# Performance work log

Measured on AMD Instinct MI355X. Metric: run time of the kernel, lower is better.

The kernel has to match this reference:

```python
import jax, jax.numpy as jnp
import numpy as np
import math
from itertools import permutations

B, C_IN, C_OUT, K, N, D, F_DIM = 2, 4, 8, 4, 224, 2, 128


def _make_perms(k):
    # [k!, k, k] permutation matrices, same ordering as itertools.permutations
    nP = math.factorial(k)
    perms = np.zeros((nP, k, k), dtype=np.float32)
    for c, p in enumerate(permutations(range(k))):
        perms[c, np.arange(k), np.array(p)] = 1.0
    return jnp.asarray(perms)


def setup_inputs() -> dict:
    key = jax.random.key(0)
    ks = jax.random.split(key, 6)
    graph = jax.random.normal(ks[0], (B, C_IN, N, N), jnp.float32)
    types = jax.random.normal(ks[1], (B, C_IN, N), jnp.float32)
    features = jax.random.normal(ks[2], (B, N, F_DIM), jnp.float32)
    # xavier-uniform-ish scales for the learned kernels
    k_struct = jax.random.normal(ks[3], (C_OUT, C_IN, K, K), jnp.float32) * 0.3
    k_row = jax.random.normal(ks[4], (C_OUT, C_IN, K), jnp.float32) * 0.5
    k_col = jax.random.normal(ks[5], (C_OUT, C_IN, K), jnp.float32) * 0.5
    return {"graph": graph, "types": types, "features": features,
            "k_struct": k_struct, "k_row": k_row, "k_col": k_col}


def _forward(graph, types, features, k_struct, k_row, k_col):
    Bn, C, Nn, _ = graph.shape
    k = k_struct.shape[-1]
    new_k = (k - 1) * D + 1
    nH = Nn - new_k + 1            # square graph -> nW == nH
    n_sub = nH * nH
    idx = jnp.arange(nH)[:, None] + jnp.arange(k) * D  # [nH, k] dilated window indices

    # --- _prepare: dilated subgraph extraction (vectorized gather) ---
    g = graph[:, :, idx, :]            # [B,C,nH,k,N]
    g = g[..., idx]                    # [B,C,nH,k,nH,k]
    sub = jnp.transpose(g, (0, 2, 4, 1, 3, 5)).reshape(Bn, n_sub, C, k, k)
    rt = jnp.transpose(types[:, :, idx], (0, 2, 1, 3))  # [B,nH,C,k]
    row_t = jnp.broadcast_to(rt[:, :, None], (Bn, nH, nH, C, k)).reshape(Bn, n_sub, C, k)
    col_t = jnp.broadcast_to(rt[:, None, :], (Bn, nH, nH, C, k)).reshape(Bn, n_sub, C, k)
    rf = features[:, idx, :].sum(axis=-2)              # [B,nH,F]
    feats = rf[:, :, None, :] + rf[:, None, :, :]      # row_features + col_features
    h_mean = feats.reshape(Bn, n_sub, -1).mean(axis=1)  # [B,F]

    # --- permuted kernels ---
    perms = _make_perms(k)                                  # [P,k,k]
    Kp = jnp.einsum('pau,oiuv,pbv->oipab', perms, k_struct, perms)  # P K P^T
    Rp = jnp.einsum('pau,oiu->oipa', perms, k_row)
    Cp = jnp.einsum('pau,oiu->oipa', perms, k_col)

    subf = sub.reshape(-1, C, k, k)   # [n,i,a,b], n = B*n_sub
    rtf = row_t.reshape(-1, C, k)
    ctf = col_t.reshape(-1, C, k)

    # ||X - Y||_F^2 = ||X||^2 + ||Y||^2 - 2<X,Y>, avoids the huge broadcasted diff
    def sq_dist(x2_ni, y2_opi, cross_nopi):
        return y2_opi[None] + x2_ni[:, None, None, :] - 2.0 * cross_nopi

    G2 = jnp.sum(subf * subf, axis=(-2, -1))                       # [n,i]
    K2 = jnp.transpose(jnp.sum(Kp * Kp, axis=(-2, -1)), (0, 2, 1))  # [o,p,i]
    struct = sq_dist(G2, K2, jnp.einsum('niab,oipab->nopi', subf, Kp))
    R2 = jnp.transpose(jnp.sum(Rp * Rp, axis=-1), (0, 2, 1))
    rsim = sq_dist(jnp.sum(rtf * rtf, axis=-1), R2, jnp.einsum('nia,oipa->nopi', rtf, Rp))
    C2 = jnp.transpose(jnp.sum(Cp * Cp, axis=-1), (0, 2, 1))
    csim = sq_dist(jnp.sum(ctf * ctf, axis=-1), C2, jnp.einsum('nia,oipa->nopi', ctf, Cp))

    total = struct + rsim + csim            # [n, o, P, i]
    # maxpool over P of (-total), negated back == min over permutations of total
    pooled = jnp.min(total, axis=2)         # [n, o, i]
    sims = jnp.transpose(pooled.reshape(Bn, n_sub, -1), (0, 2, 1))  # [B, o*i, n_sub]
    out_sim = (1.0 - jax.nn.softmax(sims, axis=-1)) / sims.shape[-1]
    return h_mean, out_sim


def reference(graph, types, features, k_struct, k_row, k_col):
    return _forward(graph, types, features, k_struct, k_row, k_col)
```

## Files before the change

kernel.cpp:

```cpp
#include <hip/hip_runtime.h>
#include <hip/hip_bf16.h>

#define B_    2
#define CIN   4
#define COUT  8
#define KK    4
#define DD    2
#define NN    224
#define FDIM  128
#define NH    218
#define NSUB  (NH*NH)
#define NPERM 24
#define NROWS (B_*COUT*CIN)
#define NSUB4 (NSUB/4)
#define CH4   512
#define MB    ((NSUB4 + CH4 - 1) / CH4)
#define OG    2

__device__ static constexpr int PERM[NPERM][4] = {
  {0,1,2,3},{0,1,3,2},{0,2,1,3},{0,2,3,1},{0,3,1,2},{0,3,2,1},
  {1,0,2,3},{1,0,3,2},{1,2,0,3},{1,2,3,0},{1,3,0,2},{1,3,2,0},
  {2,0,1,3},{2,0,3,1},{2,1,0,3},{2,1,3,0},{2,3,0,1},{2,3,1,0},
  {3,0,1,2},{3,0,2,1},{3,1,0,2},{3,1,2,0},{3,2,0,1},{3,2,1,0}
};

__global__ __launch_bounds__(64) void hmean_kernel(const float* __restrict__ features,
                                                   float* __restrict__ out) {
  int bf = blockIdx.x;
  int b = bf / FDIM, f = bf - b * FDIM;
  int lane = threadIdx.x;
  const float* fb = features + (size_t)b * NN * FDIM + f;
  float acc = 0.f;
  for (int r = lane; r < NN; r += 64) {
    int w = 0;
#pragma unroll
    for (int a = 0; a < KK; ++a) {
      int i0 = r - a * DD;
      if (0 <= i0 && i0 < NH) w++;
    }
    acc += (float)w * fb[(size_t)r * FDIM];
  }
#pragma unroll
  for (int off = 32; off > 0; off >>= 1) acc += __shfl_down(acc, off, 64);
  if (lane == 0) out[bf] = acc * (2.0f / (float)NH);
}

__global__ __launch_bounds__(256) void sims_kernel(
    const float* __restrict__ graph, const float* __restrict__ types,
    const float* __restrict__ ksA, const float* __restrict__ krA,
    const float* __restrict__ kcA, float* __restrict__ simsOut)
{
  __shared__ float ls[COUT * CIN * 16];
  __shared__ float lr[COUT * CIN * 4];
  __shared__ float lc[COUT * CIN * 4];
  __shared__ float lK2[COUT * CIN];
  int t = threadIdx.x;
  for (int i = t; i < COUT * CIN * 16; i += 256) ls[i] = ksA[i];
  for (int i = t; i < COUT * CIN * 4; i += 256) { lr[i] = krA[i]; lc[i] = kcA[i]; }
  __syncthreads();
  if (t < COUT * CIN) {
    float k2 = 0.f;
#pragma unroll
    for (int u = 0; u < 16; ++u) k2 += ls[t * 16 + u] * ls[t * 16 + u];
#pragma unroll
    for (int u = 0; u < 4; ++u) k2 += lr[t * 4 + u] * lr[t * 4 + u] + lc[t * 4 + u] * lc[t * 4 + u];
    lK2[t] = k2;
  }
  __syncthreads();

  int s = blockIdx.x * 256 + t;
  if (s >= NSUB) return;
  int yi  = blockIdx.y;
  int og  = yi >> 3;
  int bci = yi & 7;
  int b   = bci >> 2;
  int ci  = bci & 3;
  int ii  = s / NH;
  int jj  = s - ii * NH;

  const float* gi = graph + ((size_t)b * CIN + ci) * NN * NN;
  const float* ti = types + ((size_t)b * CIN + ci) * NN;

  float subv[16], rtv[4], ctv[4];
  float G2 = 0.f, T2r = 0.f, T2c = 0.f;
#pragma unroll
  for (int a = 0; a < KK; ++a) {
    const float* row = gi + (size_t)(ii + a * DD) * NN + jj;
#pragma unroll
    for (int bb = 0; bb < KK; ++bb) {
      float v = row[bb * DD];
      subv[a * 4 + bb] = v;
      G2 += v * v;
    }
    float rv = ti[ii + a * DD];
    float cv = ti[jj + a * DD];
    rtv[a] = rv; ctv[a] = cv;
    T2r += rv * rv; T2c += cv * cv;
  }
  float base0 = G2 + T2r + T2c;

#pragma unroll
  for (int oo = 0; oo < COUT / OG; ++oo) {
    int o = og * (COUT / OG) + oo;
    int oc = o * CIN + ci;
    const float* pS = ls + oc * 16;
    const float* pR = lr + oc * 4;
    const float* pC = lc + oc * 4;
    float kS[16], kR[4], kC[4];
#pragma unroll
    for (int u = 0; u < 16; ++u) kS[u] = pS[u];
#pragma unroll
    for (int u = 0; u < 4; ++u) { kR[u] = pR[u]; kC[u] = pC[u]; }

    float C1[16];
#pragma unroll
    for (int a = 0; a < 4; ++a)
#pragma unroll
      for (int ap = 0; ap < 4; ++ap)
        C1[a * 4 + ap] = subv[a * 4 + a] * kS[ap * 4 + ap]
                       + rtv[a] * kR[ap] + ctv[a] * kC[ap];

    float maxcr = -3.4e38f;
#pragma unroll
    for (int p = 0; p < NPERM; ++p) {
      const int p0 = PERM[p][0], p1 = PERM[p][1], p2 = PERM[p][2], p3 = PERM[p][3];
      float cr = C1[0 * 4 + p0] + C1[1 * 4 + p1] + C1[2 * 4 + p2] + C1[3 * 4 + p3];
      cr += subv[0*4+1] * kS[p0*4+p1];
      cr += subv[0*4+2] * kS[p0*4+p2];
      cr += subv[0*4+3] * kS[p0*4+p3];
      cr += subv[1*4+0] * kS[p1*4+p0];
      cr += subv[1*4+2] * kS[p1*4+p2];
      cr += subv[1*4+3] * kS[p1*4+p3];
      cr += subv[2*4+0] * kS[p2*4+p0];
      cr += subv[2*4+1] * kS[p2*4+p1];
      cr += subv[2*4+3] * kS[p2*4+p3];
      cr += subv[3*4+0] * kS[p3*4+p0];
      cr += subv[3*4+1] * kS[p3*4+p1];
      cr += subv[3*4+2] * kS[p3*4+p2];
      maxcr = fmaxf(maxcr, cr);
    }
    float best = base0 + lK2[oc] - 2.0f * maxcr;
    simsOut[(((size_t)b * COUT + o) * CIN + ci) * NSUB + s] = best;
  }
}

__global__ __launch_bounds__(256) void softmax_partial(const float* __restrict__ sims,
                                                       float* __restrict__ partial) {
  int blk = blockIdx.x;
  int row = blk / MB;
  int ch  = blk - row * MB;
  int base4 = ch * CH4;
  int n4 = NSUB4 - base4; if (n4 > CH4) n4 = CH4;
  const float4* rp = (const float4*)(sims + (size_t)row * NSUB) + base4;
  int t = threadIdx.x;

  float4 v[2]; int cnt = 0;
  for (int i = t; i < n4; i += 256) v[cnt++] = rp[i];

  __shared__ float red[256];
  float m = -3.4e38f;
  for (int u = 0; u < cnt; ++u)
    m = fmaxf(fmaxf(fmaxf(m, v[u].x), fmaxf(v[u].y, v[u].z)), v[u].w);
  red[t] = m; __syncthreads();
  for (int off = 128; off > 0; off >>= 1) {
    if (t < off) red[t] = fmaxf(red[t], red[t + off]);
    __syncthreads();
  }
  m = red[0]; __syncthreads();
  float l = 0.f;
  for (int u = 0; u < cnt; ++u)
    l += __expf(v[u].x - m) + __expf(v[u].y - m) + __expf(v[u].z - m) + __expf(v[u].w - m);
  red[t] = l; __syncthreads();
  for (int off = 128; off > 0; off >>= 1) {
    if (t < off) red[t] += red[t + off];
    __syncthreads();
  }
  if (t == 0) { partial[2 * blk] = m; partial[2 * blk + 1] = red[0]; }
}

__global__ __launch_bounds__(64) void softmax_combine(const float* __restrict__ partial,
                                                      float* __restrict__ stats) {
  int row = blockIdx.x;
  int t = threadIdx.x;
  float m = -3.4e38f, l = 0.f;
  if (t < MB) { m = partial[2 * (row * MB + t)]; l = partial[2 * (row * MB + t) + 1]; }
#pragma unroll
  for (int off = 32; off > 0; off >>= 1) m = fmaxf(m, __shfl_down(m, off, 64));
  m = __shfl(m, 0, 64);
  float contrib = (t < MB) ? l * __expf(partial[2 * (row * MB + t)] - m) : 0.f;
#pragma unroll
  for (int off = 32; off > 0; off >>= 1) contrib += __shfl_down(contrib, off, 64);
  if (t == 0) { stats[2 * row] = m; stats[2 * row + 1] = 1.0f / contrib; }
}

__global__ __launch_bounds__(256) void softmax_final(float* __restrict__ sims,
                                                     const float* __restrict__ stats) {
  int blk = blockIdx.x;
  int row = blk / MB;
  int ch  = blk - row * MB;
  int base4 = ch * CH4;
  int n4 = NSUB4 - base4; if (n4 > CH4) n4 = CH4;
  float4* rp = (float4*)(sims + (size_t)row * NSUB) + base4;
  float M = stats[2 * row], invS = stats[2 * row + 1];
  const float scale = 1.0f / (float)NSUB;
  for (int i = threadIdx.x; i < n4; i += 256) {
    float4 v = rp[i];
    v.x = (1.0f - __expf(v.x - M) * invS) * scale;
    v.y = (1.0f - __expf(v.y - M) * invS) * scale;
    v.z = (1.0f - __expf(v.z - M) * invS) * scale;
    v.w = (1.0f - __expf(v.w - M) * invS) * scale;
    rp[i] = v;
  }
}

extern "C" void kernel_launch(void* const* d_in, const int* in_sizes, int n_in,
                              void* d_out, int out_size, void* d_ws, size_t ws_size,
                              hipStream_t stream) {
  const float* graph    = (const float*)d_in[0];
  const float* types    = (const float*)d_in[1];
  const float* features = (const float*)d_in[2];
  const float* ks       = (const float*)d_in[3];
  const float* kr       = (const float*)d_in[4];
  const float* kc       = (const float*)d_in[5];
  float* out  = (float*)d_out;
  float* sims = out + B_ * FDIM;

  float* partial = (float*)d_ws;
  float* stats   = partial + NROWS * MB * 2;

  hmean_kernel<<<B_ * FDIM, 64, 0, stream>>>(features, out);
  dim3 sgrid((NSUB + 255) / 256, B_ * CIN * OG);
  sims_kernel<<<sgrid, 256, 0, stream>>>(graph, types, ks, kr, kc, sims);
  softmax_partial<<<NROWS * MB, 256, 0, stream>>>(sims, partial);
  softmax_combine<<<NROWS, 64, 0, stream>>>(partial, stats);
  softmax_final<<<NROWS * MB, 256, 0, stream>>>(sims, stats);
}
```

Before: 121.7 us.

## Fuse softmax partial max/sum reduction into sims kernel epilogue

Each sims block now computes its per-row block max and sum of exponentials with wave shuffles and shared memory, and writes them as partials. This removes the separate softmax_partial pass, which re-read the whole sims array. softmax_combine now merges up to 187 chunk partials with an online-softmax tree. The cost is several block barriers per output channel inside the hot loop, which is no longer unrolled, and out-of-range threads are kept alive to take part in them.

```diff
diff --git a/kernel.cpp b/kernel.cpp
--- a/kernel.cpp
+++ b/kernel.cpp
@@ -16,6 +16,8 @@
 #define CH4   512
 #define MB    ((NSUB4 + CH4 - 1) / CH4)
 #define OG    2
+#define NCHUNK ((NSUB + 255) / 256)
+#define NEGBIG (-3.4e38f)
 
 __device__ static constexpr int PERM[NPERM][4] = {
   {0,1,2,3},{0,1,3,2},{0,2,1,3},{0,2,3,1},{0,3,1,2},{0,3,2,1},
@@ -48,12 +50,14 @@
 __global__ __launch_bounds__(256) void sims_kernel(
     const float* __restrict__ graph, const float* __restrict__ types,
     const float* __restrict__ ksA, const float* __restrict__ krA,
-    const float* __restrict__ kcA, float* __restrict__ simsOut)
+    const float* __restrict__ kcA, float* __restrict__ simsOut,
+    float* __restrict__ partial)
 {
   __shared__ float ls[COUT * CIN * 16];
   __shared__ float lr[COUT * CIN * 4];
   __shared__ float lc[COUT * CIN * 4];
   __shared__ float lK2[COUT * CIN];
+  __shared__ float red[4 * 4];
   int t = threadIdx.x;
   for (int i = t; i < COUT * CIN * 16; i += 256) ls[i] = ksA[i];
   for (int i = t; i < COUT * CIN * 4; i += 256) { lr[i] = krA[i]; lc[i] = kcA[i]; }
@@ -68,8 +72,9 @@
   }
   __syncthreads();
 
-  int s = blockIdx.x * 256 + t;
-  if (s >= NSUB) return;
+  int s_raw = blockIdx.x * 256 + t;
+  bool valid = (s_raw < NSUB);
+  int s = valid ? s_raw : (NSUB - 1);
   int yi  = blockIdx.y;
   int og  = yi >> 3;
   int bci = yi & 7;
@@ -99,7 +104,9 @@
   }
   float base0 = G2 + T2r + T2c;
 
-#pragma unroll
+  int wave = t >> 6, lane = t & 63;
+
+#pragma unroll 1
   for (int oo = 0; oo < COUT / OG; ++oo) {
     int o = og * (COUT / OG) + oo;
     int oc = o * CIN + ci;
@@ -120,7 +127,7 @@
         C1[a * 4 + ap] = subv[a * 4 + a] * kS[ap * 4 + ap]
                        + rtv[a] * kR[ap] + ctv[a] * kC[ap];
 
-    float maxcr = -3.4e38f;
+    float maxcr = NEGBIG;
 #pragma unroll
     for (int p = 0; p < NPERM; ++p) {
       const int p0 = PERM[p][0], p1 = PERM[p][1], p2 = PERM[p][2], p3 = PERM[p][3];
@@ -140,57 +147,54 @@
       maxcr = fmaxf(maxcr, cr);
     }
     float best = base0 + lK2[oc] - 2.0f * maxcr;
-    simsOut[(((size_t)b * COUT + o) * CIN + ci) * NSUB + s] = best;
-  }
-}
-
-__global__ __launch_bounds__(256) void softmax_partial(const float* __restrict__ sims,
-                                                       float* __restrict__ partial) {
-  int blk = blockIdx.x;
-  int row = blk / MB;
-  int ch  = blk - row * MB;
-  int base4 = ch * CH4;
-  int n4 = NSUB4 - base4; if (n4 > CH4) n4 = CH4;
-  const float4* rp = (const float4*)(sims + (size_t)row * NSUB) + base4;
-  int t = threadIdx.x;
-
-  float4 v[2]; int cnt = 0;
-  for (int i = t; i < n4; i += 256) v[cnt++] = rp[i];
-
-  __shared__ float red[256];
-  float m = -3.4e38f;
-  for (int u = 0; u < cnt; ++u)
-    m = fmaxf(fmaxf(fmaxf(m, v[u].x), fmaxf(v[u].y, v[u].z)), v[u].w);
-  red[t] = m; __syncthreads();
-  for (int off = 128; off > 0; off >>= 1) {
-    if (t < off) red[t] = fmaxf(red[t], red[t + off]);
-    __syncthreads();
-  }
-  m = red[0]; __syncthreads();
-  float l = 0.f;
-  for (int u = 0; u < cnt; ++u)
-    l += __expf(v[u].x - m) + __expf(v[u].y - m) + __expf(v[u].z - m) + __expf(v[u].w - m);
-  red[t] = l; __syncthreads();
-  for (int off = 128; off > 0; off >>= 1) {
-    if (t < off) red[t] += red[t + off];
-    __syncthreads();
-  }
-  if (t == 0) { partial[2 * blk] = m; partial[2 * blk + 1] = red[0]; }
-}
-
-__global__ __launch_bounds__(64) void softmax_combine(const float* __restrict__ partial,
-                                                      float* __restrict__ stats) {
+    if (valid)
+      simsOut[(((size_t)b * COUT + o) * CIN + ci) * NSUB + s] = best;
+
+    float bm = valid ? best : NEGBIG;
+    float m = bm;
+#pragma unroll
+    for (int off = 32; off > 0; off >>= 1) m = fmaxf(m, __shfl_down(m, off, 64));
+    if (lane == 0) red[wave] = m;
+    __syncthreads();
+    float m_blk = fmaxf(fmaxf(red[0], red[1]), fmaxf(red[2], red[3]));
+    float e = valid ? __expf(bm - m_blk) : 0.f;
+#pragma unroll
+    for (int off = 32; off > 0; off >>= 1) e += __shfl_down(e, off, 64);
+    __syncthreads();
+    if (lane == 0) red[4 + wave] = e;
+    __syncthreads();
+    if (t == 0) {
+      float l_blk = red[4] + red[5] + red[6] + red[7];
+      int rowc = (((b * COUT + o) * CIN + ci) * NCHUNK + blockIdx.x) * 2;
+      partial[rowc]     = m_blk;
+      partial[rowc + 1] = l_blk;
+    }
+    __syncthreads();
+  }
+}
+
+__global__ __launch_bounds__(256) void softmax_combine(const float* __restrict__ partial,
+                                                       float* __restrict__ stats) {
   int row = blockIdx.x;
   int t = threadIdx.x;
-  float m = -3.4e38f, l = 0.f;
-  if (t < MB) { m = partial[2 * (row * MB + t)]; l = partial[2 * (row * MB + t) + 1]; }
-#pragma unroll
-  for (int off = 32; off > 0; off >>= 1) m = fmaxf(m, __shfl_down(m, off, 64));
-  m = __shfl(m, 0, 64);
-  float contrib = (t < MB) ? l * __expf(partial[2 * (row * MB + t)] - m) : 0.f;
-#pragma unroll
-  for (int off = 32; off > 0; off >>= 1) contrib += __shfl_down(contrib, off, 64);
-  if (t == 0) { stats[2 * row] = m; stats[2 * row + 1] = 1.0f / contrib; }
+  float m = NEGBIG, l = 0.f;
+  if (t < NCHUNK) {
+    m = partial[(row * NCHUNK + t) * 2];
+    l = partial[(row * NCHUNK + t) * 2 + 1];
+  }
+  __shared__ float ms[256], lsum[256];
+  ms[t] = m; lsum[t] = l;
+  __syncthreads();
+  for (int off = 128; off > 0; off >>= 1) {
+    if (t < off) {
+      float m2 = ms[t + off], l2 = lsum[t + off];
+      float M = fmaxf(ms[t], m2);
+      lsum[t] = lsum[t] * __expf(ms[t] - M) + l2 * __expf(m2 - M);
+      ms[t] = M;
+    }
+    __syncthreads();
+  }
+  if (t == 0) { stats[2 * row] = ms[0]; stats[2 * row + 1] = 1.0f / lsum[0]; }
 }
 
 __global__ __launch_bounds__(256) void softmax_final(float* __restrict__ sims,
@@ -226,12 +230,11 @@
   float* sims = out + B_ * FDIM;
 
   float* partial = (float*)d_ws;
-  float* stats   = partial + NROWS * MB * 2;
+  float* stats   = partial + NROWS * NCHUNK * 2;
 
   hmean_kernel<<<B_ * FDIM, 64, 0, stream>>>(features, out);
-  dim3 sgrid((NSUB + 255) / 256, B_ * CIN * OG);
-  sims_kernel<<<sgrid, 256, 0, stream>>>(graph, types, ks, kr, kc, sims);
-  softmax_partial<<<NROWS * MB, 256, 0, stream>>>(sims, partial);
-  softmax_combine<<<NROWS, 64, 0, stream>>>(partial, stats);
+  dim3 sgrid(NCHUNK, B_ * CIN * OG);
+  sims_kernel<<<sgrid, 256, 0, stream>>>(graph, types, ks, kr, kc, sims, partial);
+  softmax_combine<<<NROWS, 256, 0, stream>>>(partial, stats);
   softmax_final<<<NROWS * MB, 256, 0, stream>>>(sims, stats);
 }
```

Result: no change. 122.0 us (+0.2%).
